# Optimization experiments

Hardware: AMD Instinct MI355X
Metric: run time of the kernel (lower is better)

## Reference

```python
import jax, jax.numpy as jnp
import numpy as np

B = 32
C = 768
NH = 12
HD = C // NH
P = 16
IMG = 224
G = IMG // P           # 14 patches per side
NP = G * G             # 196 patches
DEPTH = 12
PRUNE = [1, 1, 1, 1, 0.5, 0.5, 0.5, 0.5, 0.5, 0.5, 0.5, 0.5]
MOM = 0.5              # momentum for global class-attention update
TRADE = 0.5            # slow-fast tradeoff for placeholder token update
SCALE = HD ** -0.5
NCLS = 1000

def _ln(x, g, b, eps=1e-6):
    mu = jnp.mean(x, -1, keepdims=True)
    var = jnp.mean((x - mu) ** 2, -1, keepdims=True)
    return (x - mu) * jax.lax.rsqrt(var + eps) * g + b

def setup_inputs():
    key = jax.random.key(0)
    ks = iter(jax.random.split(key, 40))
    def rn(shape, s=0.02):
        return jax.random.normal(next(ks), shape, jnp.float32) * s
    return {
        'x_img': jax.random.normal(next(ks), (B, 3, IMG, IMG), jnp.float32),
        'cls_token': rn((1, 1, C)),
        'pos_embed': rn((1, NP + 1, C)),
        'patch_w': rn((3 * P * P, C)),
        'patch_b': rn((C,)),
        'ln1_g': jnp.ones((DEPTH, C), jnp.float32),
        'ln1_b': jnp.zeros((DEPTH, C), jnp.float32),
        'qk_w': rn((DEPTH, C, 2 * C)),
        'qk_b': rn((DEPTH, 2 * C)),
        'v_w': rn((DEPTH, C, C)),
        'v_b': rn((DEPTH, C)),
        'proj_w': rn((DEPTH, C, C)),
        'proj_b': rn((DEPTH, C)),
        'ln2_g': jnp.ones((DEPTH, C), jnp.float32),
        'ln2_b': jnp.zeros((DEPTH, C), jnp.float32),
        'fc1_w': rn((DEPTH, C, 4 * C)),
        'fc1_b': rn((DEPTH, 4 * C)),
        'fc2_w': rn((DEPTH, 4 * C, C)),
        'fc2_b': rn((DEPTH, C)),
        'norm_g': jnp.ones((C,), jnp.float32),
        'norm_b': jnp.zeros((C,), jnp.float32),
        'head_w': rn((C, NCLS)),
        'head_b': rn((NCLS,)),
    }

def reference(x_img, cls_token, pos_embed, patch_w, patch_b, ln1_g, ln1_b,
              qk_w, qk_b, v_w, v_b, proj_w, proj_b, ln2_g, ln2_b,
              fc1_w, fc1_b, fc2_w, fc2_b, norm_g, norm_b, head_w, head_b):
    Bq = x_img.shape[0]
    # PatchEmbed: Conv2d(k=P, stride=P) == flatten each patch as (c, ph, pw) then matmul
    patches = x_img.reshape(Bq, 3, G, P, G, P).transpose(0, 2, 4, 1, 3, 5)
    patches = patches.reshape(Bq, NP, 3 * P * P)
    x = patches @ patch_w + patch_b                                   # [B,196,C]
    x = jnp.concatenate([jnp.broadcast_to(cls_token, (Bq, 1, C)), x], 1)
    x = x + pos_embed                                                 # [B,197,C]

    def block(xt, i):
        # QKAttention + VAttention + proj residual, then MlpBlock residual.
        t = _ln(xt, ln1_g[i], ln1_b[i])
        Nt = t.shape[1]
        qk = (t @ qk_w[i] + qk_b[i]).reshape(Bq, Nt, 2, NH, HD)
        q = qk[:, :, 0].transpose(0, 2, 1, 3)                         # [B,H,Nt,hd]
        k = qk[:, :, 1].transpose(0, 2, 1, 3)
        attn = jax.nn.softmax(jnp.einsum('bhnd,bhmd->bhnm', q, k) * SCALE, -1)
        v = (t @ v_w[i] + v_b[i]).reshape(Bq, Nt, NH, HD).transpose(0, 2, 1, 3)
        o = jnp.einsum('bhnm,bhmd->bhnd', attn, v).transpose(0, 2, 1, 3).reshape(Bq, Nt, C)
        xt = xt + (o @ proj_w[i] + proj_b[i])
        h = _ln(xt, ln2_g[i], ln2_b[i])
        xt = xt + (jax.nn.gelu(h @ fc1_w[i] + fc1_b[i], approximate=False) @ fc2_w[i] + fc2_b[i])
        row = attn[:, :, 0, 1:].sum(1)   # cls-attention row, summed over heads
        return xt, row

    cls_attn = None
    for i in range(DEPTH):
        if PRUNE[i] == 1:
            x, row = block(x, i)
            cls_attn = row if cls_attn is None else (1 - MOM) * cls_attn + MOM * row
        else:
            N_ = int(NP * PRUNE[i])                        # informative token count
            idx = jnp.argsort(-cls_attn, axis=1)           # sort patches by score (easy_gather)
            xp = jnp.take_along_axis(x[:, 1:], idx[:, :, None], axis=1)
            cls_attn = jnp.take_along_axis(cls_attn, idx, axis=1)
            fast = xp[:, N_:]                              # placeholder (pruned) tokens
            score = cls_attn[:, N_:]
            rep = (fast * score[:, :, None]).sum(1, keepdims=True) \
                  / score.sum(1, keepdims=True)[:, :, None]  # representative token
            xs = jnp.concatenate([x[:, :1], xp[:, :N_], rep], 1)   # [B,N_+2,C]
            xs, row = block(xs, i)
            cls_attn = jnp.concatenate(
                [(1 - MOM) * cls_attn[:, :N_] + MOM * row[:, :N_], cls_attn[:, N_:]], 1)
            fast = fast + TRADE * (xs[:, -1:] - rep)       # fast update via rep residual
            x = jnp.concatenate([xs[:, :N_ + 1], fast], 1)  # back to [B,197,C]

    x = _ln(x, norm_g, norm_b)
    return x[:, 0] @ head_w + head_b                        # [B,1000]
```

## Files before the change

kernel.cpp:

```cpp
#include <hip/hip_runtime.h>
#include <hip/hip_bf16.h>
#include <stdint.h>

#define B_ 32
#define C_ 768
#define NH_ 12
#define HD_ 64
#define NP_ 196
#define NTOK 197
#define NKEEP 98
#define NCLS_ 1000
#define MPAD 6400
#define RS_ (3 * C_)

typedef __bf16 bf16x8 __attribute__((ext_vector_type(8)));
typedef float f32x4 __attribute__((ext_vector_type(4)));

__device__ __forceinline__ float blockReduceSum256(float v) {
    __shared__ float red[4];
    const int lane = threadIdx.x & 63, w = threadIdx.x >> 6;
#pragma unroll
    for (int off = 32; off; off >>= 1) v += __shfl_down(v, off);
    __syncthreads();
    if (lane == 0) red[w] = v;
    __syncthreads();
    return red[0] + red[1] + red[2] + red[3];
}

__device__ __forceinline__ void gload16(void* lds, const void* g) {
    __builtin_amdgcn_global_load_lds(
        (const __attribute__((address_space(1))) void*)g,
        (__attribute__((address_space(3))) void*)lds,
        16, 0, 0);
}

__global__ __launch_bounds__(256) void patchify_kernel(const float* __restrict__ img,
                                                       __hip_bfloat16* __restrict__ patches)
{
    const int bp = blockIdx.x;
    const int b = bp / NP_, p = bp % NP_;
    const int gy = p / 14, gx = p % 14;
    const int tid = threadIdx.x;
#pragma unroll
    for (int j = 0; j < 3; ++j) {
        const int e = tid + j * 256;
        const int c = e >> 8, rem = e & 255, py = rem >> 4, px = rem & 15;
        patches[(size_t)bp * C_ + e] = __float2bfloat16(
            img[(((size_t)b * 3 + c) * 224 + gy * 16 + py) * 224 + gx * 16 + px]);
    }
}

__global__ __launch_bounds__(256) void assemble_x_kernel(const float* __restrict__ pemb,
                                                         const float* __restrict__ cls_tok,
                                                         const float* __restrict__ pos,
                                                         float* __restrict__ x)
{
    const int b = blockIdx.x, t = blockIdx.y, tid = threadIdx.x;
#pragma unroll
    for (int j = 0; j < 3; ++j) {
        const int c = tid + j * 256;
        const float v = (t == 0) ? cls_tok[c] : pemb[((size_t)b * NP_ + (t - 1)) * C_ + c];
        x[((size_t)b * NTOK + t) * C_ + c] = v + pos[(size_t)t * C_ + c];
    }
}

__global__ __launch_bounds__(256) void ln_kernel(const float* __restrict__ x,
                                                 const float* __restrict__ g,
                                                 const float* __restrict__ b,
                                                 __hip_bfloat16* outB, float* outF,
                                                 long long inRowStride, int nRows)
{
    const int row = (blockIdx.x << 2) + (threadIdx.x >> 6);
    const int lane = threadIdx.x & 63;
    if (row >= nRows) return;
    const float* xr = x + (size_t)row * inRowStride;
    float4 v0 = *(const float4*)(xr + (lane << 2));
    float4 v1 = *(const float4*)(xr + 256 + (lane << 2));
    float4 v2 = *(const float4*)(xr + 512 + (lane << 2));
    float s = v0.x + v0.y + v0.z + v0.w + v1.x + v1.y + v1.z + v1.w
            + v2.x + v2.y + v2.z + v2.w;
#pragma unroll
    for (int off = 1; off < 64; off <<= 1) s += __shfl_xor(s, off);
    const float mu = s * (1.f / C_);
    float q = 0.f;
    {
        float d;
        d = v0.x - mu; q += d * d; d = v0.y - mu; q += d * d;
        d = v0.z - mu; q += d * d; d = v0.w - mu; q += d * d;
        d = v1.x - mu; q += d * d; d = v1.y - mu; q += d * d;
        d = v1.z - mu; q += d * d; d = v1.w - mu; q += d * d;
        d = v2.x - mu; q += d * d; d = v2.y - mu; q += d * d;
        d = v2.z - mu; q += d * d; d = v2.w - mu; q += d * d;
    }
#pragma unroll
    for (int off = 1; off < 64; off <<= 1) q += __shfl_xor(q, off);
    const float rs = rsqrtf(q * (1.f / C_) + 1e-6f);
    const float4 vv[3] = {v0, v1, v2};
#pragma unroll
    for (int j = 0; j < 3; ++j) {
        const int cbase = (j << 8) + (lane << 2);
        const float4 gv = *(const float4*)(g + cbase);
        const float4 bv = *(const float4*)(b + cbase);
        float o0 = (vv[j].x - mu) * rs * gv.x + bv.x;
        float o1 = (vv[j].y - mu) * rs * gv.y + bv.y;
        float o2 = (vv[j].z - mu) * rs * gv.z + bv.z;
        float o3 = (vv[j].w - mu) * rs * gv.w + bv.w;
        if (outB) {
            union { unsigned short us[4]; uint2 u; } pk;
            __hip_bfloat16 h;
            h = __float2bfloat16(o0); pk.us[0] = *(unsigned short*)&h;
            h = __float2bfloat16(o1); pk.us[1] = *(unsigned short*)&h;
            h = __float2bfloat16(o2); pk.us[2] = *(unsigned short*)&h;
            h = __float2bfloat16(o3); pk.us[3] = *(unsigned short*)&h;
            *(uint2*)((unsigned short*)outB + (size_t)row * C_ + cbase) = pk.u;
        }
        if (outF) {
            float4 o; o.x = o0; o.y = o1; o.z = o2; o.w = o3;
            *(float4*)(outF + (size_t)row * C_ + cbase) = o;
        }
    }
}

__global__ __launch_bounds__(256) void transpose_bf16_kernel(const float* __restrict__ W,
                                                             __hip_bfloat16* __restrict__ Wt,
                                                             int K, int N,
                                                             long long outLstride, long long outOff)
{
    __shared__ float tile[32][33];
    const size_t loffIn = (size_t)blockIdx.z * K * N;
    const size_t loffOut = (size_t)blockIdx.z * outLstride + outOff;
    const int k0 = blockIdx.y << 5, n0 = blockIdx.x << 5;
    const int tid = threadIdx.x;
#pragma unroll
    for (int e = tid; e < 1024; e += 256) {
        const int r = e >> 5, c = e & 31;
        tile[r][c] = W[loffIn + (size_t)(k0 + r) * N + n0 + c];
    }
    __syncthreads();
#pragma unroll
    for (int e = tid; e < 1024; e += 256) {
        const int r = e >> 5, c = e & 31;
        Wt[loffOut + (size_t)(n0 + r) * K + k0 + c] = __float2bfloat16(tile[c][r]);
    }
}

__global__ __launch_bounds__(256) void concat_bias_kernel(const float* __restrict__ qk_b,
                                                          const float* __restrict__ v_b,
                                                          float* __restrict__ out)
{
    const int i = blockIdx.x * 256 + threadIdx.x;
    if (i < 12 * RS_) {
        const int l = i / RS_, c = i % RS_;
        out[i] = (c < 2 * C_) ? qk_b[l * 2 * C_ + c] : v_b[l * C_ + (c - 2 * C_)];
    }
}

template<int GELU, int OMODE>
__global__ __launch_bounds__(256, 4) void gemm_bf16_kernel(const __hip_bfloat16* __restrict__ A,
                                                           const __hip_bfloat16* __restrict__ Bt,
                                                           const float* __restrict__ bias,
                                                           const float* __restrict__ res,
                                                           float* __restrict__ outF,
                                                           __hip_bfloat16* __restrict__ outB,
                                                           int K, int N)
{
    __shared__ __align__(16) unsigned short sMem[16384];
    const int tid = threadIdx.x;
    const int wv = tid >> 6, ln = tid & 63;

    const int nwg = gridDim.x * gridDim.y;
    int lid = blockIdx.y * gridDim.x + blockIdx.x;
    {
        const int q = nwg >> 3, r = nwg & 7;
        const int xcd = lid & 7, lq = lid >> 3;
        lid = (xcd < r ? xcd * (q + 1) : r * (q + 1) + (xcd - r) * q) + lq;
    }
    const int bn = (lid % gridDim.x) << 7;
    const int bm = (lid / gridDim.x) << 7;

    const int wr = wv >> 1, wc = wv & 1;
    const int ln15 = ln & 15, lhi = ln >> 4;

    int offA[2], offB[2];
#pragma unroll
    for (int i = 0; i < 2; ++i) {
        const int s = (i << 8) + tid;
        const int L = s >> 3, cp = (s & 7) ^ (L & 7);
        offA[i] = (bm + (L << 1) + (cp >> 2)) * K + ((cp & 3) << 3);
        offB[i] = (bn + (L << 1) + (cp >> 2)) * K + ((cp & 3) << 3);
    }

    const unsigned ldsBase =
        (unsigned)(size_t)(__attribute__((address_space(3))) unsigned short*)&sMem[0];
    unsigned aOff[4], bOff[4];
#pragma unroll
    for (int m = 0; m < 4; ++m) {
        const int r = (wr << 6) + (m << 4) + ln15;
        const int L = r >> 1;
        const int pc = (((r & 1) << 2) + lhi) ^ (L & 7);
        aOff[m] = (unsigned)((L << 7) + (pc << 4));
    }
#pragma unroll
    for (int n = 0; n < 4; ++n) {
        const int r = (wc << 6) + (n << 4) + ln15;
        const int L = r >> 1;
        const int pc = (((r & 1) << 2) + lhi) ^ (L & 7);
        bOff[n] = (unsigned)(8192 + (L << 7) + (pc << 4));
    }

    f32x4 acc[4][4] = {};

    auto stage = [&](int bufByte, int kt) {
        const int k0 = kt << 5;
        unsigned short* base = sMem + (bufByte >> 1);
        gload16(base + ((0 * 256 + (wv << 6)) << 3), A + offA[0] + k0);
        gload16(base + ((1 * 256 + (wv << 6)) << 3), A + offA[1] + k0);
        gload16(base + 4096 + ((0 * 256 + (wv << 6)) << 3), Bt + offB[0] + k0);
        gload16(base + 4096 + ((1 * 256 + (wv << 6)) << 3), Bt + offB[1] + k0);
    };
    auto compute = [&](unsigned bufOff) {
        bf16x8 a[4], b[4];
#pragma unroll
        for (int m = 0; m < 4; ++m)
            asm volatile("ds_read_b128 %0, %1" : "=v"(a[m]) : "v"(ldsBase + bufOff + aOff[m]));
#pragma unroll
        for (int n = 0; n < 4; ++n)
            asm volatile("ds_read_b128 %0, %1" : "=v"(b[n]) : "v"(ldsBase + bufOff + bOff[n]));
        asm volatile("s_waitcnt lgkmcnt(0)" ::: "memory");
        __builtin_amdgcn_sched_barrier(0);
#pragma unroll
        for (int m = 0; m < 4; ++m)
#pragma unroll
            for (int n = 0; n < 4; ++n)
                acc[m][n] = __builtin_amdgcn_mfma_f32_16x16x32_bf16(a[m], b[n], acc[m][n], 0, 0, 0);
    };

    const int ntiles = K >> 5;
    stage(0, 0);
    asm volatile("s_waitcnt vmcnt(0)" ::: "memory");
    __builtin_amdgcn_s_barrier();
    int t = 0;
    for (; t + 2 < ntiles; t += 2) {
        stage(16384, t + 1);
        asm volatile("s_waitcnt vmcnt(4)" ::: "memory");
        __builtin_amdgcn_s_barrier();
        compute(0u);
        __builtin_amdgcn_s_barrier();
        stage(0, t + 2);
        asm volatile("s_waitcnt vmcnt(4)" ::: "memory");
        __builtin_amdgcn_s_barrier();
        compute(16384u);
        __builtin_amdgcn_s_barrier();
    }
    stage(16384, ntiles - 1);
    asm volatile("s_waitcnt vmcnt(4)" ::: "memory");
    __builtin_amdgcn_s_barrier();
    compute(0u);
    __builtin_amdgcn_s_barrier();
    asm volatile("s_waitcnt vmcnt(0)" ::: "memory");
    __builtin_amdgcn_s_barrier();
    compute(16384u);
    __syncthreads();

    if (OMODE == 0) {
        unsigned short* sOut = sMem;
#pragma unroll
        for (int n = 0; n < 4; ++n) {
            const int col = (wc << 6) + (n << 4) + ln15;
            const float bv = bias[bn + col];
#pragma unroll
            for (int m = 0; m < 4; ++m) {
                const int row0 = (wr << 6) + (m << 4) + (lhi << 2);
#pragma unroll
                for (int r = 0; r < 4; ++r) {
                    float x = acc[m][n][r] + bv;
                    if (GELU) x = 0.5f * x * (1.f + erff(x * 0.70710678118654752f));
                    const __hip_bfloat16 hb = __float2bfloat16(x);
                    sOut[(row0 + r) * 128 + col] = *(const unsigned short*)&hb;
                }
            }
        }
        __syncthreads();
#pragma unroll
        for (int i = 0; i < 8; ++i) {
            const int chunk = (i << 8) + tid;
            const int row = chunk >> 4, c8 = (chunk & 15) << 3;
            *(uint4*)((unsigned short*)outB + (size_t)(bm + row) * N + bn + c8) =
                *(const uint4*)(sOut + row * 128 + c8);
        }
    } else {
#pragma unroll
        for (int n = 0; n < 4; ++n) {
            const int gcn = bn + (wc << 6) + (n << 4) + ln15;
            const float bv = bias[gcn];
#pragma unroll
            for (int m = 0; m < 4; ++m) {
                const int gr0 = bm + (wr << 6) + (m << 4) + (lhi << 2);
                f32x4 v = acc[m][n];
#pragma unroll
                for (int r = 0; r < 4; ++r) {
                    const size_t o = (size_t)(gr0 + r) * N + gcn;
                    float x = v[r] + bv;
                    if (OMODE == 1) x += res[o];
                    outF[o] = x;
                }
            }
        }
    }
}

template<int OMODE>
__global__ __launch_bounds__(256, 4) void gemm_half_kernel(const __hip_bfloat16* __restrict__ A,
                                                           const __hip_bfloat16* __restrict__ Bt,
                                                           const float* __restrict__ bias,
                                                           const float* __restrict__ res,
                                                           float* __restrict__ outF,
                                                           int K, int N)
{
    __shared__ __align__(16) unsigned short sMem[3 * 6144];
    const int tid = threadIdx.x;
    const int wv = tid >> 6, ln = tid & 63;

    const int nwg = gridDim.x * gridDim.y;
    int lid = blockIdx.y * gridDim.x + blockIdx.x;
    {
        const int q = nwg >> 3, r = nwg & 7;
        const int xcd = lid & 7, lq = lid >> 3;
        lid = (xcd < r ? xcd * (q + 1) : r * (q + 1) + (xcd - r) * q) + lq;
    }
    const int bn = (lid % gridDim.x) << 7;
    const int bm = (lid / gridDim.x) << 6;

    const int wr = wv >> 1, wc = wv & 1;
    const int ln15 = ln & 15, lhi = ln >> 4;

    int offA, offB[2];
    {
        const int L = tid >> 3, cp = (tid & 7) ^ (L & 7);
        offA = (bm + (L << 1) + (cp >> 2)) * K + ((cp & 3) << 3);
    }
#pragma unroll
    for (int i = 0; i < 2; ++i) {
        const int s = (i << 8) + tid;
        const int L = s >> 3, cp = (s & 7) ^ (L & 7);
        offB[i] = (bn + (L << 1) + (cp >> 2)) * K + ((cp & 3) << 3);
    }

    const unsigned ldsBase =
        (unsigned)(size_t)(__attribute__((address_space(3))) unsigned short*)&sMem[0];
    unsigned aOff[2], bOff[4];
#pragma unroll
    for (int m = 0; m < 2; ++m) {
        const int r = (wr << 5) + (m << 4) + ln15;
        const int L = r >> 1;
        const int pc = (((r & 1) << 2) + lhi) ^ (L & 7);
        aOff[m] = (unsigned)((L << 7) + (pc << 4));
    }
#pragma unroll
    for (int n = 0; n < 4; ++n) {
        const int r = (wc << 6) + (n << 4) + ln15;
        const int L = r >> 1;
        const int pc = (((r & 1) << 2) + lhi) ^ (L & 7);
        bOff[n] = (unsigned)(4096 + (L << 7) + (pc << 4));
    }

    f32x4 acc[2][4] = {};

    auto stage = [&](int bufUShort, int kt) {
        const int k0 = kt << 5;
        unsigned short* base = sMem + bufUShort;
        gload16(base + ((wv << 6) << 3), A + offA + k0);
        gload16(base + 2048 + ((0 * 256 + (wv << 6)) << 3), Bt + offB[0] + k0);
        gload16(base + 2048 + ((1 * 256 + (wv << 6)) << 3), Bt + offB[1] + k0);
    };
    auto compute = [&](unsigned bufByte) {
        bf16x8 a[2], b[4];
#pragma unroll
        for (int m = 0; m < 2; ++m)
            asm volatile("ds_read_b128 %0, %1" : "=v"(a[m]) : "v"(ldsBase + bufByte + aOff[m]));
#pragma unroll
        for (int n = 0; n < 4; ++n)
            asm volatile("ds_read_b128 %0, %1" : "=v"(b[n]) : "v"(ldsBase + bufByte + bOff[n]));
        asm volatile("s_waitcnt lgkmcnt(0)" ::: "memory");
        __builtin_amdgcn_sched_barrier(0);
#pragma unroll
        for (int m = 0; m < 2; ++m)
#pragma unroll
            for (int n = 0; n < 4; ++n)
                acc[m][n] = __builtin_amdgcn_mfma_f32_16x16x32_bf16(a[m], b[n], acc[m][n], 0, 0, 0);
    };

    const int ntiles = K >> 5;
    stage(0, 0);
    stage(6144, 1);
    int t = 0;
    for (; t + 3 < ntiles; t += 3) {
        asm volatile("s_waitcnt vmcnt(3)" ::: "memory");
        __builtin_amdgcn_s_barrier();
        stage(12288, t + 2);
        compute(0u);
        asm volatile("s_waitcnt vmcnt(3)" ::: "memory");
        __builtin_amdgcn_s_barrier();
        stage(0, t + 3);
        compute(12288u);
        asm volatile("s_waitcnt vmcnt(3)" ::: "memory");
        __builtin_amdgcn_s_barrier();
        stage(6144, t + 4);
        compute(24576u);
    }
    asm volatile("s_waitcnt vmcnt(3)" ::: "memory");
    __builtin_amdgcn_s_barrier();
    stage(12288, t + 2);
    compute(0u);
    asm volatile("s_waitcnt vmcnt(3)" ::: "memory");
    __builtin_amdgcn_s_barrier();
    compute(12288u);
    asm volatile("s_waitcnt vmcnt(0)" ::: "memory");
    __builtin_amdgcn_s_barrier();
    compute(24576u);

#pragma unroll
    for (int n = 0; n < 4; ++n) {
        const int gcn = bn + (wc << 6) + (n << 4) + ln15;
        const float bv = bias[gcn];
#pragma unroll
        for (int m = 0; m < 2; ++m) {
            const int gr0 = bm + (wr << 5) + (m << 4) + (lhi << 2);
            f32x4 v = acc[m][n];
#pragma unroll
            for (int r = 0; r < 4; ++r) {
                const size_t o = (size_t)(gr0 + r) * N + gcn;
                float x = v[r] + bv;
                if (OMODE == 1) x += res[o];
                outF[o] = x;
            }
        }
    }
}

__global__ __launch_bounds__(256) void head_kernel(const float* __restrict__ A,
                                                   const float* __restrict__ W,
                                                   const float* __restrict__ bias,
                                                   float* __restrict__ out)
{
    const int n = blockIdx.x * 256 + threadIdx.x;
    const int m = blockIdx.y;
    if (n >= NCLS_) return;
    const float* a = A + (size_t)m * C_;
    float s = 0.f;
#pragma unroll 8
    for (int k = 0; k < C_; ++k) s = fmaf(a[k], W[(size_t)k * NCLS_ + n], s);
    out[(size_t)m * NCLS_ + n] = s + bias[n];
}

template<int NT16>
__global__ __launch_bounds__(256) void attn_mfma_kernel(const __hip_bfloat16* __restrict__ qkv,
                                                        __hip_bfloat16* __restrict__ o,
                                                        float* __restrict__ attn0,
                                                        int Nt)
{
    constexpr int NPAD = NT16 * 16;
    constexpr int PSW = (((NPAD / 8) & 7) == 0) ? 7 : 3;
    constexpr int VSW = 7;
    constexpr int PROWB = NPAD * 2 + 16;
    constexpr int VROWB = (NPAD == 224) ? 528 : 272;
    __shared__ unsigned short sK[NPAD * 64 + 512];
    __shared__ unsigned short sV[32 * VROWB];

    const int bh = blockIdx.x;
    const int b = bh / NH_, h = bh % NH_;
    const int qtile = blockIdx.y;
    const int tid = threadIdx.x, ln = tid & 63, wv = tid >> 6;
    const int ln15 = ln & 15, lhi = ln >> 4;
    const __hip_bfloat16* qkbase = qkv + (size_t)b * Nt * RS_;

#pragma unroll
    for (int it = 0; it < NPAD * 8 / 256; ++it) {
        const int p = it * 256 + tid;
        int key = p >> 3;
        const int c = (p & 7) ^ (key & 7);
        if (key >= Nt) key = Nt - 1;
        unsigned short* dst = sK + (size_t)(it * 256 + (wv << 6)) * 8;
        gload16(dst, qkbase + (size_t)key * RS_ + C_ + (h << 6) + (c << 3));
    }
#pragma unroll
    for (int it = 0; it < NPAD * 8 / 256; ++it) {
        const int e = it * 256 + tid;
        const int key = e >> 3, dc = e & 7;
        union { uint4 u; unsigned short us[8]; } val;
        val.u = make_uint4(0u, 0u, 0u, 0u);
        if (key < Nt)
            val.u = *(const uint4*)(qkbase + (size_t)key * RS_ + 2 * C_ + (h << 6) + (dc << 3));
        const int kc = key >> 3, kb = (key & 7) << 1;
#pragma unroll
        for (int j = 0; j < 8; ++j) {
            const int d = (dc << 3) + j;
            *(unsigned short*)((char*)sV + d * VROWB + ((kc ^ ((d >> 3) & VSW)) << 4) + kb) = val.us[j];
        }
    }
    const int qbase = qtile * 64 + (wv << 4);
    int qrow = qbase + ln15; if (qrow >= Nt) qrow = Nt - 1;
    const __hip_bfloat16* qp = qkbase + (size_t)qrow * RS_ + (h << 6) + (lhi << 3);
    const bf16x8 qf0 = *(const bf16x8*)qp;
    const bf16x8 qf1 = *(const bf16x8*)(qp + 32);
    __syncthreads();

    f32x4 sc[NT16];
#pragma unroll
    for (int t = 0; t < NT16; ++t) {
        const int key = (t << 4) + ln15;
        const unsigned short* kr = sK + (size_t)key * 64;
        const bf16x8 k0 = *(const bf16x8*)(kr + ((lhi ^ (key & 7)) << 3));
        const bf16x8 k1 = *(const bf16x8*)(kr + (((4 + lhi) ^ (key & 7)) << 3));
        f32x4 a = {0.f, 0.f, 0.f, 0.f};
        a = __builtin_amdgcn_mfma_f32_16x16x32_bf16(k0, qf0, a, 0, 0, 0);
        a = __builtin_amdgcn_mfma_f32_16x16x32_bf16(k1, qf1, a, 0, 0, 0);
        sc[t] = a;
    }
    __syncthreads();

    float mx = -1e30f;
#pragma unroll
    for (int t = 0; t < NT16; ++t)
#pragma unroll
        for (int r = 0; r < 4; ++r) {
            const int key = (t << 4) + (lhi << 2) + r;
            const float v = (key < Nt) ? sc[t][r] * 0.125f : -1e30f;
            sc[t][r] = v;
            mx = fmaxf(mx, v);
        }
    mx = fmaxf(mx, __shfl_xor(mx, 16));
    mx = fmaxf(mx, __shfl_xor(mx, 32));
    float sum = 0.f;
#pragma unroll
    for (int t = 0; t < NT16; ++t)
#pragma unroll
        for (int r = 0; r < 4; ++r) {
            const float e = expf(sc[t][r] - mx);
            sc[t][r] = e; sum += e;
        }
    sum += __shfl_xor(sum, 16);
    sum += __shfl_xor(sum, 32);
    const float inv = 1.f / sum;

    char* Pw = (char*)sK + wv * (16 * PROWB);
    const bool isQ0 = (qtile == 0) && (wv == 0) && (ln15 == 0);
#pragma unroll
    for (int t = 0; t < NT16; ++t) {
        union { unsigned short us[4]; uint2 u2; } pk;
#pragma unroll
        for (int r = 0; r < 4; ++r) {
            const float p = sc[t][r] * inv;
            const __hip_bfloat16 hb = __float2bfloat16(p);
            pk.us[r] = *(const unsigned short*)&hb;
            if (isQ0) {
                const int key = (t << 4) + (lhi << 2) + r;
                if (key < Nt) attn0[(size_t)bh * NTOK + key] = p;
            }
        }
        const int chunk = ((t << 1) + (lhi >> 1)) ^ (ln15 & PSW);
        *(uint2*)(Pw + ln15 * PROWB + (chunk << 4) + ((lhi & 1) << 3)) = pk.u2;
    }
    __syncthreads();

    f32x4 oa[4] = {};
#pragma unroll
    for (int s = 0; s < NPAD / 32; ++s) {
        const bf16x8 pf = *(const bf16x8*)(Pw + ln15 * PROWB +
                                           ((((s << 2) + lhi) ^ (ln15 & PSW)) << 4));
#pragma unroll
        for (int n = 0; n < 4; ++n) {
            const int d = (n << 4) + ln15;
            const bf16x8 vf = *(const bf16x8*)((char*)sV + d * VROWB +
                                               ((((s << 2) + lhi) ^ ((d >> 3) & VSW)) << 4));
            oa[n] = __builtin_amdgcn_mfma_f32_16x16x32_bf16(pf, vf, oa[n], 0, 0, 0);
        }
    }
#pragma unroll
    for (int n = 0; n < 4; ++n)
#pragma unroll
        for (int r = 0; r < 4; ++r) {
            const int qq = qbase + (lhi << 2) + r;
            if (qq < Nt)
                o[((size_t)b * Nt + qq) * C_ + (h << 6) + (n << 4) + ln15] =
                    __float2bfloat16(oa[n][r]);
        }
}

__global__ __launch_bounds__(256) void row_cls_ema_kernel(const float* __restrict__ attn0,
                                                          float* __restrict__ cls, int first)
{
    const int b = blockIdx.x, t = threadIdx.x;
    if (t < NP_) {
        float s = 0.f;
#pragma unroll
        for (int h = 0; h < NH_; ++h) s += attn0[((size_t)(b * NH_ + h)) * NTOK + 1 + t];
        const int i = b * NP_ + t;
        cls[i] = first ? s : 0.5f * cls[i] + 0.5f * s;
    }
}

__global__ __launch_bounds__(256) void row_cls_prune_kernel(const float* __restrict__ attn0,
                                                            const float* __restrict__ sorted,
                                                            float* __restrict__ cls)
{
    const int b = blockIdx.x, t = threadIdx.x;
    if (t < NP_) {
        float sv = sorted[b * NP_ + t];
        if (t < NKEEP) {
            float s = 0.f;
#pragma unroll
            for (int h = 0; h < NH_; ++h) s += attn0[((size_t)(b * NH_ + h)) * NTOK + 1 + t];
            sv = 0.5f * sv + 0.5f * s;
        }
        cls[b * NP_ + t] = sv;
    }
}

__global__ __launch_bounds__(256) void rank_kernel(const float* __restrict__ cls,
                                                   int* __restrict__ idx,
                                                   float* __restrict__ sorted,
                                                   float* __restrict__ ssum)
{
    __shared__ float sv[NP_];
    const int b = blockIdx.x, t = threadIdx.x;
    if (t < NP_) sv[t] = cls[b * NP_ + t];
    __syncthreads();
    float val = 0.f; int r = NP_;
    if (t < NP_) {
        val = sv[t];
        r = 0;
        for (int j = 0; j < NP_; ++j) {
            const float vj = sv[j];
            r += (vj > val || (vj == val && j < t)) ? 1 : 0;
        }
        idx[b * NP_ + r] = t;
        sorted[b * NP_ + r] = val;
    }
    const float contrib = (t < NP_ && r >= NKEEP) ? val : 0.f;
    const float tot = blockReduceSum256(contrib);
    if (t == 0) ssum[b] = tot;
}

__global__ __launch_bounds__(256) void build_xs_kernel(const float* __restrict__ x,
                                                       const int* __restrict__ idx,
                                                       const float* __restrict__ sorted,
                                                       const float* __restrict__ ssum,
                                                       float* __restrict__ xs,
                                                       float* __restrict__ fast,
                                                       float* __restrict__ rep,
                                                       const float* __restrict__ lng,
                                                       const float* __restrict__ lnb,
                                                       __hip_bfloat16* __restrict__ tb)
{
    const int b = blockIdx.x, t = blockIdx.y, tid = threadIdx.x;
    const float* xb = x + (size_t)b * NTOK * C_;

    float v0, v1, v2;
    int ldsRow = -1;

    if (t == 0) {
        v0 = xb[tid]; v1 = xb[tid + 256]; v2 = xb[tid + 512];
        ldsRow = 0;
    } else if (t <= NKEEP) {
        const int src = 1 + idx[b * NP_ + (t - 1)];
        const float* xr = xb + (size_t)src * C_;
        v0 = xr[tid]; v1 = xr[tid + 256]; v2 = xr[tid + 512];
        ldsRow = t;
    } else if (t == NKEEP + 1) {
        const float inv = 1.f / ssum[b];
        float a0 = 0.f, a1 = 0.f, a2 = 0.f;
        for (int jj = 0; jj < NP_ - NKEEP; ++jj) {
            const int src = 1 + idx[b * NP_ + NKEEP + jj];
            const float wgt = sorted[b * NP_ + NKEEP + jj];
            const float* xr = xb + (size_t)src * C_;
            a0 = fmaf(xr[tid], wgt, a0);
            a1 = fmaf(xr[tid + 256], wgt, a1);
            a2 = fmaf(xr[tid + 512], wgt, a2);
        }
        v0 = a0 * inv; v1 = a1 * inv; v2 = a2 * inv;
        rep[(size_t)b * C_ + tid] = v0;
        rep[(size_t)b * C_ + tid + 256] = v1;
        rep[(size_t)b * C_ + tid + 512] = v2;
        ldsRow = 99;
    } else {
        const int jf = t - (NKEEP + 2);
        const int src = 1 + idx[b * NP_ + NKEEP + jf];
#pragma unroll
        for (int j = 0; j < 3; ++j) {
            const int c = tid + j * 256;
            fast[((size_t)b * (NP_ - NKEEP) + jf) * C_ + c] = xb[(size_t)src * C_ + c];
        }
        return;
    }

    float* xsr = xs + ((size_t)b * 100 + ldsRow) * C_;
    xsr[tid] = v0; xsr[tid + 256] = v1; xsr[tid + 512] = v2;

    const float mu = blockReduceSum256(v0 + v1 + v2) * (1.f / C_);
    const float d0 = v0 - mu, d1 = v1 - mu, d2 = v2 - mu;
    const float var = blockReduceSum256(d0 * d0 + d1 * d1 + d2 * d2) * (1.f / C_);
    const float rs = rsqrtf(var + 1e-6f);
    __hip_bfloat16* tr = tb + ((size_t)b * 100 + ldsRow) * C_;
    tr[tid]       = __float2bfloat16(d0 * rs * lng[tid]       + lnb[tid]);
    tr[tid + 256] = __float2bfloat16(d1 * rs * lng[tid + 256] + lnb[tid + 256]);
    tr[tid + 512] = __float2bfloat16(d2 * rs * lng[tid + 512] + lnb[tid + 512]);
}

__global__ __launch_bounds__(256) void scatter_back_kernel(const float* __restrict__ xs,
                                                           const float* __restrict__ fast,
                                                           const float* __restrict__ rep,
                                                           float* __restrict__ x)
{
    const int b = blockIdx.x, t = blockIdx.y, tid = threadIdx.x;
#pragma unroll
    for (int j = 0; j < 3; ++j) {
        const int c = tid + j * 256;
        float v;
        if (t <= NKEEP)
            v = xs[((size_t)b * 100 + t) * C_ + c];
        else
            v = fast[((size_t)b * (NP_ - NKEEP) + (t - NKEEP - 1)) * C_ + c]
                + 0.5f * (xs[((size_t)b * 100 + 99) * C_ + c] - rep[(size_t)b * C_ + c]);
        x[((size_t)b * NTOK + t) * C_ + c] = v;
    }
}

extern "C" void kernel_launch(void* const* d_in, const int* in_sizes, int n_in,
                              void* d_out, int out_size, void* d_ws, size_t ws_size,
                              hipStream_t stream)
{
    (void)in_sizes; (void)n_in; (void)out_size;
    const float* x_img   = (const float*)d_in[0];
    const float* cls_tok = (const float*)d_in[1];
    const float* pos     = (const float*)d_in[2];
    const float* patch_w = (const float*)d_in[3];
    const float* patch_b = (const float*)d_in[4];
    const float* ln1_g   = (const float*)d_in[5];
    const float* ln1_b   = (const float*)d_in[6];
    const float* qk_w    = (const float*)d_in[7];
    const float* qk_b    = (const float*)d_in[8];
    const float* v_w     = (const float*)d_in[9];
    const float* v_b     = (const float*)d_in[10];
    const float* proj_w  = (const float*)d_in[11];
    const float* proj_b  = (const float*)d_in[12];
    const float* ln2_g   = (const float*)d_in[13];
    const float* ln2_b   = (const float*)d_in[14];
    const float* fc1_w   = (const float*)d_in[15];
    const float* fc1_b   = (const float*)d_in[16];
    const float* fc2_w   = (const float*)d_in[17];
    const float* fc2_b   = (const float*)d_in[18];
    const float* norm_g  = (const float*)d_in[19];
    const float* norm_b  = (const float*)d_in[20];
    const float* head_w  = (const float*)d_in[21];
    const float* head_b  = (const float*)d_in[22];

    char* base = (char*)d_ws;
    size_t off = 0;
    auto alloc = [&](size_t bytes) -> void* {
        void* p = base + off; off = (off + bytes + 255) & ~(size_t)255; return p;
    };
    float* X    = (float*)alloc((size_t)MPAD * C_ * 4);
    __hip_bfloat16* Tb   = (__hip_bfloat16*)alloc((size_t)MPAD * C_ * 2);
    __hip_bfloat16* QKVb = (__hip_bfloat16*)alloc((size_t)MPAD * RS_ * 2);
    __hip_bfloat16* Hb   = (__hip_bfloat16*)alloc((size_t)MPAD * 4 * C_ * 2);
    float* XS   = (float*)alloc((size_t)3200 * C_ * 4);
    float* FAST = (float*)alloc((size_t)B_ * (NP_ - NKEEP) * C_ * 4);
    float* REP  = (float*)alloc((size_t)B_ * C_ * 4);
    float* ATTN0= (float*)alloc((size_t)B_ * NH_ * NTOK * 4);
    float* CLS  = (float*)alloc((size_t)B_ * NP_ * 4);
    float* SORT = (float*)alloc((size_t)B_ * NP_ * 4);
    float* SSUM = (float*)alloc((size_t)B_ * 4);
    float* T0   = (float*)alloc((size_t)B_ * C_ * 4);
    int*   IDX  = (int*)alloc((size_t)B_ * NP_ * 4);
    float* BIASQKV = (float*)alloc((size_t)12 * RS_ * 4);
    __hip_bfloat16* WTpatch = (__hip_bfloat16*)alloc((size_t)C_ * C_ * 2);
    __hip_bfloat16* WTqkv   = (__hip_bfloat16*)alloc((size_t)12 * RS_ * C_ * 2);
    __hip_bfloat16* WTproj  = (__hip_bfloat16*)alloc((size_t)12 * C_ * C_ * 2);
    __hip_bfloat16* WTfc1   = (__hip_bfloat16*)alloc((size_t)12 * C_ * 4 * C_ * 2);
    __hip_bfloat16* WTfc2   = (__hip_bfloat16*)alloc((size_t)12 * 4 * C_ * C_ * 2);
    if (off > ws_size) return;

    __hip_bfloat16* Ob    = Hb;
    __hip_bfloat16* PATCH = Hb;
    float*          PEMB  = (float*)QKVb;

    const dim3 blk(256);

    transpose_bf16_kernel<<<dim3(24, 24, 1), blk, 0, stream>>>(patch_w, WTpatch, C_, C_, (long long)C_ * C_, 0);
    transpose_bf16_kernel<<<dim3(48, 24, 12), blk, 0, stream>>>(qk_w, WTqkv, C_, 2 * C_, (long long)RS_ * C_, 0);
    transpose_bf16_kernel<<<dim3(24, 24, 12), blk, 0, stream>>>(v_w, WTqkv, C_, C_, (long long)RS_ * C_, (long long)2 * C_ * C_);
    transpose_bf16_kernel<<<dim3(24, 24, 12), blk, 0, stream>>>(proj_w, WTproj, C_, C_, (long long)C_ * C_, 0);
    transpose_bf16_kernel<<<dim3(96, 24, 12), blk, 0, stream>>>(fc1_w, WTfc1, C_, 4 * C_, (long long)4 * C_ * C_, 0);
    transpose_bf16_kernel<<<dim3(24, 96, 12), blk, 0, stream>>>(fc2_w, WTfc2, 4 * C_, C_, (long long)4 * C_ * C_, 0);
    concat_bias_kernel<<<(12 * RS_ + 255) / 256, blk, 0, stream>>>(qk_b, v_b, BIASQKV);

    auto runBlock = [&](int i, float* xb, int Nt, bool skipLn1) {
        const int M = B_ * Nt;
        const int mt = (M + 127) >> 7;
        const int mt64 = (M + 63) >> 6;
        const int qtiles = (Nt + 63) >> 6;
        if (!skipLn1)
            ln_kernel<<<(M + 3) / 4, blk, 0, stream>>>(xb, ln1_g + i * C_, ln1_b + i * C_, Tb, nullptr, C_, M);
        gemm_bf16_kernel<0, 0><<<dim3(RS_ / 128, mt), blk, 0, stream>>>(
            Tb, WTqkv + (size_t)i * RS_ * C_, BIASQKV + (size_t)i * RS_, nullptr, nullptr, QKVb, C_, RS_);
        if (Nt == NTOK)
            attn_mfma_kernel<14><<<dim3(B_ * NH_, qtiles), blk, 0, stream>>>(QKVb, Ob, ATTN0, Nt);
        else
            attn_mfma_kernel<8><<<dim3(B_ * NH_, qtiles), blk, 0, stream>>>(QKVb, Ob, ATTN0, Nt);
        gemm_half_kernel<1><<<dim3(6, mt64), blk, 0, stream>>>(
            Ob, WTproj + (size_t)i * C_ * C_, proj_b + (size_t)i * C_, xb, xb, C_, C_);
        ln_kernel<<<(M + 3) / 4, blk, 0, stream>>>(xb, ln2_g + i * C_, ln2_b + i * C_, Tb, nullptr, C_, M);
        gemm_bf16_kernel<1, 0><<<dim3(24, mt), blk, 0, stream>>>(
            Tb, WTfc1 + (size_t)i * C_ * 4 * C_, fc1_b + (size_t)i * 4 * C_, nullptr, nullptr, Hb, C_, 4 * C_);
        gemm_half_kernel<1><<<dim3(6, mt64), blk, 0, stream>>>(
            Hb, WTfc2 + (size_t)i * 4 * C_ * C_, fc2_b + (size_t)i * C_, xb, xb, 4 * C_, C_);
    };

    patchify_kernel<<<B_ * NP_, blk, 0, stream>>>(x_img, PATCH);
    gemm_half_kernel<2><<<dim3(6, 98), blk, 0, stream>>>(
        PATCH, WTpatch, patch_b, nullptr, PEMB, C_, C_);
    assemble_x_kernel<<<dim3(B_, NTOK), blk, 0, stream>>>(PEMB, cls_tok, pos, X);

    for (int i = 0; i < 12; ++i) {
        if (i < 4) {
            runBlock(i, X, NTOK, false);
            row_cls_ema_kernel<<<B_, blk, 0, stream>>>(ATTN0, CLS, i == 0 ? 1 : 0);
        } else {
            rank_kernel<<<B_, blk, 0, stream>>>(CLS, IDX, SORT, SSUM);
            build_xs_kernel<<<dim3(B_, 198), blk, 0, stream>>>(
                X, IDX, SORT, SSUM, XS, FAST, REP, ln1_g + i * C_, ln1_b + i * C_, Tb);
            runBlock(i, XS, 100, true);
            scatter_back_kernel<<<dim3(B_, NTOK), blk, 0, stream>>>(XS, FAST, REP, X);
            row_cls_prune_kernel<<<B_, blk, 0, stream>>>(ATTN0, SORT, CLS);
        }
    }

    ln_kernel<<<8, blk, 0, stream>>>(X, norm_g, norm_b, nullptr, T0, (long long)NTOK * C_, B_);
    head_kernel<<<dim3(4, B_), blk, 0, stream>>>(T0, head_w, head_b, (float*)d_out);
}
```

Baseline: 2.461 ms.

## Deepen half-GEMM pipeline to four LDS stages with register fragment prefetch

The half-tile GEMM moves from a three-buffer to a four-buffer LDS ring. It also double-buffers the A/B fragments in registers, so the next tile's LDS reads are issued before the MFMAs run on the current tile. This hides LDS read latency behind matrix math and keeps more global loads in flight. In exchange, LDS per block rises to 48KB and register pressure grows, which may lower occupancy below the requested four blocks per CU.

Measured after the change: 2.450 ms, median of 2. About the same (-0.4%).

```diff
diff --git a/kernel.cpp b/kernel.cpp
--- a/kernel.cpp
+++ b/kernel.cpp
@@ -309,6 +309,33 @@
     }
 }
 
+#define HSTEP(VMC, PBUF, SBUF, CA, CB, NA, NB, DOSTAGE, DOPRE, KS)             \
+    {                                                                          \
+        asm volatile("s_waitcnt vmcnt(" VMC ")" ::: "memory");                 \
+        __builtin_amdgcn_s_barrier();                                          \
+        if (DOSTAGE) stage((SBUF) * 6144, (KS));                               \
+        if (DOPRE) {                                                           \
+            _Pragma("unroll")                                                  \
+            for (int m_ = 0; m_ < 2; ++m_)                                     \
+                asm volatile("ds_read_b128 %0, %1"                             \
+                    : "=v"(NA[m_]) : "v"(ldsBase + (PBUF) * 12288u + aOff[m_]));\
+            _Pragma("unroll")                                                  \
+            for (int n_ = 0; n_ < 4; ++n_)                                     \
+                asm volatile("ds_read_b128 %0, %1"                             \
+                    : "=v"(NB[n_]) : "v"(ldsBase + (PBUF) * 12288u + bOff[n_]));\
+            asm volatile("s_waitcnt lgkmcnt(6)" ::: "memory");                 \
+        } else {                                                               \
+            asm volatile("s_waitcnt lgkmcnt(0)" ::: "memory");                 \
+        }                                                                      \
+        __builtin_amdgcn_sched_barrier(0);                                     \
+        _Pragma("unroll")                                                      \
+        for (int m_ = 0; m_ < 2; ++m_)                                         \
+            _Pragma("unroll")                                                  \
+            for (int n_ = 0; n_ < 4; ++n_)                                     \
+                acc[m_][n_] = __builtin_amdgcn_mfma_f32_16x16x32_bf16(         \
+                    CA[m_], CB[n_], acc[m_][n_], 0, 0, 0);                     \
+    }
+
 template<int OMODE>
 __global__ __launch_bounds__(256, 4) void gemm_half_kernel(const __hip_bfloat16* __restrict__ A,
                                                            const __hip_bfloat16* __restrict__ Bt,
@@ -317,7 +344,7 @@
                                                            float* __restrict__ outF,
                                                            int K, int N)
 {
-    __shared__ __align__(16) unsigned short sMem[3 * 6144];
+    __shared__ __align__(16) unsigned short sMem[4 * 6144];
     const int tid = threadIdx.x;
     const int wv = tid >> 6, ln = tid & 63;
 
@@ -365,6 +392,7 @@
     }
 
     f32x4 acc[2][4] = {};
+    bf16x8 r0a[2], r0b[4], r1a[2], r1b[4];
 
     auto stage = [&](int bufUShort, int kt) {
         const int k0 = kt << 5;
@@ -373,51 +401,31 @@
         gload16(base + 2048 + ((0 * 256 + (wv << 6)) << 3), Bt + offB[0] + k0);
         gload16(base + 2048 + ((1 * 256 + (wv << 6)) << 3), Bt + offB[1] + k0);
     };
-    auto compute = [&](unsigned bufByte) {
-        bf16x8 a[2], b[4];
-#pragma unroll
-        for (int m = 0; m < 2; ++m)
-            asm volatile("ds_read_b128 %0, %1" : "=v"(a[m]) : "v"(ldsBase + bufByte + aOff[m]));
-#pragma unroll
-        for (int n = 0; n < 4; ++n)
-            asm volatile("ds_read_b128 %0, %1" : "=v"(b[n]) : "v"(ldsBase + bufByte + bOff[n]));
-        asm volatile("s_waitcnt lgkmcnt(0)" ::: "memory");
-        __builtin_amdgcn_sched_barrier(0);
-#pragma unroll
-        for (int m = 0; m < 2; ++m)
-#pragma unroll
-            for (int n = 0; n < 4; ++n)
-                acc[m][n] = __builtin_amdgcn_mfma_f32_16x16x32_bf16(a[m], b[n], acc[m][n], 0, 0, 0);
-    };
 
     const int ntiles = K >> 5;
     stage(0, 0);
     stage(6144, 1);
+    stage(12288, 2);
+    asm volatile("s_waitcnt vmcnt(6)" ::: "memory");
+    __builtin_amdgcn_s_barrier();
+#pragma unroll
+    for (int m = 0; m < 2; ++m)
+        asm volatile("ds_read_b128 %0, %1" : "=v"(r0a[m]) : "v"(ldsBase + aOff[m]));
+#pragma unroll
+    for (int n = 0; n < 4; ++n)
+        asm volatile("ds_read_b128 %0, %1" : "=v"(r0b[n]) : "v"(ldsBase + bOff[n]));
+
     int t = 0;
-    for (; t + 3 < ntiles; t += 3) {
-        asm volatile("s_waitcnt vmcnt(3)" ::: "memory");
-        __builtin_amdgcn_s_barrier();
-        stage(12288, t + 2);
-        compute(0u);
-        asm volatile("s_waitcnt vmcnt(3)" ::: "memory");
-        __builtin_amdgcn_s_barrier();
-        stage(0, t + 3);
-        compute(12288u);
-        asm volatile("s_waitcnt vmcnt(3)" ::: "memory");
-        __builtin_amdgcn_s_barrier();
-        stage(6144, t + 4);
-        compute(24576u);
-    }
-    asm volatile("s_waitcnt vmcnt(3)" ::: "memory");
-    __builtin_amdgcn_s_barrier();
-    stage(12288, t + 2);
-    compute(0u);
-    asm volatile("s_waitcnt vmcnt(3)" ::: "memory");
-    __builtin_amdgcn_s_barrier();
-    compute(12288u);
-    asm volatile("s_waitcnt vmcnt(0)" ::: "memory");
-    __builtin_amdgcn_s_barrier();
-    compute(24576u);
+    for (; t < ntiles - 4; t += 4) {
+        HSTEP("3", 1, 3, r0a, r0b, r1a, r1b, true, true, t + 3);
+        HSTEP("3", 2, 0, r1a, r1b, r0a, r0b, true, true, t + 4);
+        HSTEP("3", 3, 1, r0a, r0b, r1a, r1b, true, true, t + 5);
+        HSTEP("3", 0, 2, r1a, r1b, r0a, r0b, true, true, t + 6);
+    }
+    HSTEP("3", 1, 3, r0a, r0b, r1a, r1b, true,  true,  t + 3);
+    HSTEP("3", 2, 0, r1a, r1b, r0a, r0b, false, true,  0);
+    HSTEP("0", 3, 0, r0a, r0b, r1a, r1b, false, true,  0);
+    HSTEP("0", 0, 0, r1a, r1b, r0a, r0b, false, false, 0);
 
 #pragma unroll
     for (int n = 0; n < 4; ++n) {
```
